# Kernel tuning notes

Hardware: AMD Instinct MI355X
Metric: run time of the kernel (lower is better)

Reference implementation:

```python
import jax, jax.numpy as jnp
import numpy as np

K_HEADS = 8
D_HEAD = 64
D = K_HEADS * D_HEAD  # 512
B, TP, TQ, N = 8, 48, 48, 256


def setup_inputs() -> dict:
    key = jax.random.key(0)
    ks = jax.random.split(key, 13)
    s = 1.0 / np.sqrt(D)
    inp = {
        "X": jax.random.normal(ks[0], (B, TP, N, D), jnp.float32),
        "STE_P": jax.random.normal(ks[1], (B, TP, N, D), jnp.float32),
        "STE_Q": jax.random.normal(ks[2], (B, TQ, N, D), jnp.float32),
        "Wq": jax.random.uniform(ks[3], (D, D), jnp.float32, -s, s),
        "bq": jax.random.uniform(ks[4], (D,), jnp.float32, -s, s),
        "Wk": jax.random.uniform(ks[5], (D, D), jnp.float32, -s, s),
        "bk": jax.random.uniform(ks[6], (D,), jnp.float32, -s, s),
        "Wv": jax.random.uniform(ks[7], (D, D), jnp.float32, -s, s),
        "bv": jax.random.uniform(ks[8], (D,), jnp.float32, -s, s),
        "W1": jax.random.uniform(ks[9], (D, D), jnp.float32, -s, s),
        "b1": jax.random.uniform(ks[10], (D,), jnp.float32, -s, s),
        "W2": jax.random.uniform(ks[11], (D, D), jnp.float32, -s, s),
        "b2": jax.random.uniform(ks[12], (D,), jnp.float32, -s, s),
    }
    return inp


def reference(X, STE_P, STE_Q, Wq, bq, Wk, bk, Wv, bv, W1, b1, W2, b2):
    # ReLU-fused QKV projections
    q = jax.nn.relu(STE_Q @ Wq + bq)  # [B, Tq, N, D]
    k = jax.nn.relu(STE_P @ Wk + bk)  # [B, Tp, N, D]
    v = jax.nn.relu(X @ Wv + bv)      # [B, Tp, N, D]

    # split(last, d) + cat(dim 0) == introduce head axis h of size K
    b, tq, n, _ = q.shape
    tp = k.shape[1]
    q = q.reshape(b, tq, n, K_HEADS, D_HEAD)
    k = k.reshape(b, tp, n, K_HEADS, D_HEAD)
    v = v.reshape(b, tp, n, K_HEADS, D_HEAD)

    # attention over the TIME axis, per node and head: scores [b,h,n,tq,tp]
    scale = 1.0 / jnp.sqrt(jnp.asarray(D_HEAD, q.dtype))
    attn = jnp.einsum('bqnhd,bpnhd->bhnqp', q, k) * scale
    attn = jax.nn.softmax(attn, axis=-1)
    out = jnp.einsum('bhnqp,bpnhd->bqnhd', attn, v).reshape(b, tq, n, D)

    out = jax.nn.relu(out @ W1 + b1) @ W2 + b2
    return out
```

## Files before the change

### kernel.cpp

```cpp
#include <hip/hip_runtime.h>

typedef _Float16 f16;
typedef __fp16 hf2 __attribute__((ext_vector_type(2)));
typedef _Float16 f16x4 __attribute__((ext_vector_type(4)));
typedef _Float16 f16x8 __attribute__((ext_vector_type(8)));
typedef float f32x4 __attribute__((ext_vector_type(4)));

typedef const __attribute__((address_space(1))) unsigned int guint;
typedef __attribute__((address_space(3))) unsigned int luint;
__device__ __forceinline__ void gl_lds16(const void* g, void* l) {
    __builtin_amdgcn_global_load_lds((guint*)g, (luint*)l, 16, 0, 0);
}
template <int N>
__device__ __forceinline__ void vmwait() {
    if constexpr (N == 8)       asm volatile("s_waitcnt vmcnt(8)" ::: "memory");
    else if constexpr (N == 5)  asm volatile("s_waitcnt vmcnt(5)" ::: "memory");
    else if constexpr (N == 4)  asm volatile("s_waitcnt vmcnt(4)" ::: "memory");
    else                        asm volatile("s_waitcnt vmcnt(0)" ::: "memory");
}
__device__ __forceinline__ void barrier_raw() { __builtin_amdgcn_s_barrier(); __builtin_amdgcn_sched_barrier(0); }

__device__ __forceinline__ f16x8 pack8(float4 x0, float4 x1) {
    hf2 p0 = __builtin_amdgcn_cvt_pkrtz(x0.x, x0.y);
    hf2 p1 = __builtin_amdgcn_cvt_pkrtz(x0.z, x0.w);
    hf2 p2 = __builtin_amdgcn_cvt_pkrtz(x1.x, x1.y);
    hf2 p3 = __builtin_amdgcn_cvt_pkrtz(x1.z, x1.w);
    f16x8 h;
    h[0] = (f16)p0[0]; h[1] = (f16)p0[1]; h[2] = (f16)p1[0]; h[3] = (f16)p1[1];
    h[4] = (f16)p2[0]; h[5] = (f16)p2[1]; h[6] = (f16)p3[0]; h[7] = (f16)p3[1];
    return h;
}

__global__ __launch_bounds__(256) void wconv(const float* w0, const float* w1, const float* w2,
                                             const float* w3, const float* w4, f16* dst) {
    const float* src;
    switch (blockIdx.z) { case 0: src = w0; break; case 1: src = w1; break;
                          case 2: src = w2; break; case 3: src = w3; break; default: src = w4; }
    __shared__ float tile[32][33];
    int k0 = blockIdx.x * 32, n0 = blockIdx.y * 32;
    int t = threadIdx.x;
    int r = t >> 3, c4 = (t & 7) * 4;
    float4 v = *(const float4*)(src + (k0 + r) * 512 + n0 + c4);
    tile[r][c4 + 0] = v.x; tile[r][c4 + 1] = v.y; tile[r][c4 + 2] = v.z; tile[r][c4 + 3] = v.w;
    __syncthreads();
    f16x4 o;
    o[0] = (f16)tile[c4 + 0][r]; o[1] = (f16)tile[c4 + 1][r];
    o[2] = (f16)tile[c4 + 2][r]; o[3] = (f16)tile[c4 + 3][r];
    *(f16x4*)(dst + (size_t)blockIdx.z * 262144 + (n0 + r) * 512 + k0 + c4) = o;
}

__global__ __launch_bounds__(256) void conv3(const float* __restrict__ a0, const float* __restrict__ a1,
                                             const float* __restrict__ a2, f16* __restrict__ d0,
                                             f16* __restrict__ d1, f16* __restrict__ d2) {
    const float* s; f16* d;
    if (blockIdx.y == 0)      { s = a0; d = d0; }
    else if (blockIdx.y == 1) { s = a1; d = d1; }
    else                      { s = a2; d = d2; }
    const int n8 = 6291456;
    int i = blockIdx.x * 256 + threadIdx.x;
    const int stride = gridDim.x * 256;
    for (; i < n8; i += stride) {
        const float4* p = (const float4*)(s + (size_t)i * 8);
        float4 x0 = p[0], x1 = p[1];
        *(f16x8*)(d + (size_t)i * 8) = pack8(x0, x1);
    }
}

__global__ __launch_bounds__(512, 1) void gemm_f512(const f16* __restrict__ A,
                                                    const f16* __restrict__ Bt,
                                                    const float* __restrict__ bias,
                                                    f16* __restrict__ Cp) {
    constexpr int ASZ = 8192;
    constexpr int BSZ = 32768;
    constexpr int BUFSZ = ASZ + BSZ;
    __shared__ __align__(16) char smem[3 * BUFSZ];

    const int cpx = gridDim.x >> 3;
    const int orig = blockIdx.x;
    const int bx = (orig & 7) * cpx + (orig >> 3);
    const int r0 = bx * 128;

    const int t = threadIdx.x;
    const int j = t & 63, w = t >> 6;
    const int lr = j & 15, lq = j >> 4;
    const int wr = (w >> 2) * 64, wc = (w & 3) * 128;

    const int sblk = (t & 3) ^ ((t >> 3) & 3);
    const f16* aS = A  + (size_t)(r0 + (t >> 2)) * 512 + sblk * 8;
    const f16* bS = Bt + (size_t)(t >> 2) * 512 + sblk * 8;
    const int dstT = t * 16;

    int aoff[4], boff[8];
#pragma unroll
    for (int m = 0; m < 4; m++) {
        int row = wr + m * 16 + lr;
        aoff[m] = row * 64 + ((lq ^ ((row >> 1) & 3)) << 4);
    }
#pragma unroll
    for (int nb = 0; nb < 8; nb++) {
        int row = wc + nb * 16 + lr;
        boff[nb] = ASZ + row * 64 + ((lq ^ ((row >> 1) & 3)) << 4);
    }

    f32x4 acc[4][8] = {};

    auto stageA = [&](int kt, int buf) {
        gl_lds16(aS + kt * 32, smem + buf * BUFSZ + dstT);
    };
    auto stageB01 = [&](int kt, int buf) {
        char* d = smem + buf * BUFSZ + ASZ + dstT;
        const f16* s = bS + kt * 32;
        gl_lds16(s, d);
        gl_lds16(s + 65536, d + 8192);
    };
    auto stageB23 = [&](int kt, int buf) {
        char* d = smem + buf * BUFSZ + ASZ + dstT;
        const f16* s = bS + kt * 32;
        gl_lds16(s + 131072, d + 16384);
        gl_lds16(s + 196608, d + 24576);
    };

    stageA(0, 0); stageB01(0, 0); stageB23(0, 0);
    stageA(1, 1); stageB01(1, 1); stageB23(1, 1);

    int bufc = 0;
#pragma unroll 1
    for (int kt = 0; kt < 16; ++kt) {
        const char* sb = smem + bufc * BUFSZ;
        const int b1 = (bufc == 2) ? 0 : bufc + 1;
        const int bufs2 = (b1 == 2) ? 0 : b1 + 1;
        if (kt < 15) vmwait<5>(); else vmwait<0>();
        barrier_raw();
        if (kt < 14) { stageA(kt + 2, bufs2); stageB01(kt + 2, bufs2); }
        f16x8 bfr[8], afr[2];
#pragma unroll
        for (int nb = 0; nb < 8; nb++) bfr[nb] = *(const f16x8*)(sb + boff[nb]);
#pragma unroll
        for (int m = 0; m < 2; m++) afr[m] = *(const f16x8*)(sb + aoff[m]);
        __builtin_amdgcn_s_setprio(1);
#pragma unroll
        for (int m = 0; m < 2; m++)
#pragma unroll
            for (int nb = 0; nb < 8; nb++)
                acc[m][nb] = __builtin_amdgcn_mfma_f32_16x16x32_f16(afr[m], bfr[nb], acc[m][nb], 0, 0, 0);
        __builtin_amdgcn_s_setprio(0);
        barrier_raw();
        if (kt < 14) stageB23(kt + 2, bufs2);
        f16x8 afr2[2];
#pragma unroll
        for (int m = 0; m < 2; m++) afr2[m] = *(const f16x8*)(sb + aoff[m + 2]);
        __builtin_amdgcn_s_setprio(1);
#pragma unroll
        for (int m = 0; m < 2; m++)
#pragma unroll
            for (int nb = 0; nb < 8; nb++)
                acc[m + 2][nb] = __builtin_amdgcn_mfma_f32_16x16x32_f16(afr2[m], bfr[nb], acc[m + 2][nb], 0, 0, 0);
        __builtin_amdgcn_s_setprio(0);
        bufc = b1;
    }

#pragma unroll
    for (int nb = 0; nb < 8; nb++) {
        int col = wc + nb * 16 + lr;
        float b = bias[col];
#pragma unroll
        for (int m = 0; m < 4; m++) {
#pragma unroll
            for (int r = 0; r < 4; r++) {
                float v = fmaxf(acc[m][nb][r] + b, 0.0f);
                size_t row = (size_t)(r0 + wr + m * 16 + lq * 4 + r);
                Cp[row * 512 + col] = (f16)v;
            }
        }
    }
}

template <bool RELU, bool O16>
__global__ __launch_bounds__(512, 2) void gemm_8ph(const f16* __restrict__ A,
                                                   const f16* __restrict__ Bt,
                                                   const float* __restrict__ bias,
                                                   void* __restrict__ Cp) {
    constexpr int BUFSZ = 32768;
    __shared__ __align__(16) char smem[4 * BUFSZ];

    const int cpx = gridDim.x >> 3;
    const int orig = blockIdx.x;
    const int wgid = (orig & 7) * cpx + (orig >> 3);
    const int by = wgid & 1;
    const int bx = wgid >> 1;
    const int r0 = bx * 256, c0 = by * 256;

    const int t = threadIdx.x;
    const int j = t & 63, w = t >> 6;
    const int lr = j & 15, lq = j >> 4;
    const int wr = (w >> 2) * 128, wc = (w & 3) * 64;

    const int srow = t >> 2;
    const int sblk = (t & 3) ^ ((t >> 3) & 3);
    const f16* aS = A  + (size_t)(r0 + srow) * 512 + sblk * 8;
    const f16* bS = Bt + (size_t)(c0 + srow) * 512 + sblk * 8;
    const int dstT = t * 16;

    int aoff[8], boff[4];
#pragma unroll
    for (int m = 0; m < 8; m++) {
        int row = wr + m * 16 + lr;
        aoff[m] = row * 64 + ((lq ^ ((row >> 1) & 3)) << 4);
    }
#pragma unroll
    for (int nb = 0; nb < 4; nb++) {
        int row = wc + nb * 16 + lr;
        boff[nb] = 16384 + row * 64 + ((lq ^ ((row >> 1) & 3)) << 4);
    }

    f32x4 acc[8][4] = {};

    auto stageA = [&](int kt) {
        char* d = smem + (kt & 3) * BUFSZ + dstT;
        const f16* s = aS + kt * 32;
        gl_lds16(s, d);
        gl_lds16(s + 65536, d + 8192);
    };
    auto stageB = [&](int kt) {
        char* d = smem + (kt & 3) * BUFSZ + 16384 + dstT;
        const f16* s = bS + kt * 32;
        gl_lds16(s, d);
        gl_lds16(s + 65536, d + 8192);
    };

    stageA(0); stageB(0); stageA(1); stageB(1); stageA(2); stageB(2);

#pragma unroll 1
    for (int kt = 0; kt < 16; ++kt) {
        const char* sb = smem + (kt & 3) * BUFSZ;
        if (kt <= 13)      vmwait<8>();
        else if (kt == 14) vmwait<4>();
        else               vmwait<0>();
        barrier_raw();
        if (kt < 13) stageA(kt + 3);
        f16x8 bfr[4], afr[4];
#pragma unroll
        for (int nb = 0; nb < 4; nb++) bfr[nb] = *(const f16x8*)(sb + boff[nb]);
#pragma unroll
        for (int m = 0; m < 4; m++) afr[m] = *(const f16x8*)(sb + aoff[m]);
        __builtin_amdgcn_s_setprio(1);
#pragma unroll
        for (int m = 0; m < 4; m++)
#pragma unroll
            for (int nb = 0; nb < 4; nb++)
                acc[m][nb] = __builtin_amdgcn_mfma_f32_16x16x32_f16(afr[m], bfr[nb], acc[m][nb], 0, 0, 0);
        __builtin_amdgcn_s_setprio(0);
        barrier_raw();
        if (kt < 13) stageB(kt + 3);
        f16x8 afr2[4];
#pragma unroll
        for (int m = 0; m < 4; m++) afr2[m] = *(const f16x8*)(sb + aoff[m + 4]);
        __builtin_amdgcn_s_setprio(1);
#pragma unroll
        for (int m = 0; m < 4; m++)
#pragma unroll
            for (int nb = 0; nb < 4; nb++)
                acc[m + 4][nb] = __builtin_amdgcn_mfma_f32_16x16x32_f16(afr2[m], bfr[nb], acc[m + 4][nb], 0, 0, 0);
        __builtin_amdgcn_s_setprio(0);
    }

#pragma unroll
    for (int nb = 0; nb < 4; nb++) {
        int col = c0 + wc + nb * 16 + lr;
        float b = bias[col];
#pragma unroll
        for (int m = 0; m < 8; m++) {
#pragma unroll
            for (int r = 0; r < 4; r++) {
                float v = acc[m][nb][r] + b;
                if (RELU) v = fmaxf(v, 0.0f);
                size_t row = (size_t)(r0 + wr + m * 16 + lq * 4 + r);
                if (O16) ((f16*)Cp)[row * 512 + col] = (f16)v;
                else     ((float*)Cp)[row * 512 + col] = v;
            }
        }
    }
}

__global__ __launch_bounds__(64) void attn_kernel(const f16* __restrict__ q,
                                                  const f16* __restrict__ k,
                                                  const f16* __restrict__ v,
                                                  f16* __restrict__ out) {
    const int h = blockIdx.x, n = blockIdx.y, b = blockIdx.z;
    __shared__ f16 sQ[48 * 72];
    __shared__ f16 sK[48 * 72];
    __shared__ f16 sP[48 * 72];
    __shared__ f16 sVt[64 * 72];
    const int l = threadIdx.x, lr = l & 15, lq = l >> 4;
    const size_t rowstride = 256 * 512;
    const size_t base = ((size_t)(b * 48) * 256 + n) * 512 + h * 64;

    const int pr = l >> 3, pc = (l & 7) * 8;
#pragma unroll
    for (int pass = 0; pass < 6; pass++) {
        int row = pass * 8 + pr;
        size_t g = base + (size_t)row * rowstride + pc;
        f16x8 qv = *(const f16x8*)(q + g);
        f16x8 kv = *(const f16x8*)(k + g);
        f16x8 vv = *(const f16x8*)(v + g);
        *(f16x8*)&sQ[row * 72 + pc] = qv;
        *(f16x8*)&sK[row * 72 + pc] = kv;
#pragma unroll
        for (int jj = 0; jj < 8; jj++) sVt[(pc + jj) * 72 + row] = vv[jj];
    }
    {
        f16x8 z = {};
        *(f16x8*)&sVt[l * 72 + 48] = z;
        *(f16x8*)&sVt[l * 72 + 56] = z;
        if (l < 48) { *(f16x8*)&sP[l * 72 + 48] = z; *(f16x8*)&sP[l * 72 + 56] = z; }
    }
    __syncthreads();

    f32x4 s[3][3] = {};
#pragma unroll
    for (int ks = 0; ks < 2; ks++) {
        f16x8 aq[3], bk[3];
#pragma unroll
        for (int m = 0; m < 3; m++)  aq[m] = *(const f16x8*)&sQ[(m * 16 + lr) * 72 + ks * 32 + lq * 8];
#pragma unroll
        for (int nb = 0; nb < 3; nb++) bk[nb] = *(const f16x8*)&sK[(nb * 16 + lr) * 72 + ks * 32 + lq * 8];
#pragma unroll
        for (int m = 0; m < 3; m++)
#pragma unroll
            for (int nb = 0; nb < 3; nb++)
                s[m][nb] = __builtin_amdgcn_mfma_f32_16x16x32_f16(aq[m], bk[nb], s[m][nb], 0, 0, 0);
    }

#pragma unroll
    for (int m = 0; m < 3; m++) {
#pragma unroll
        for (int r = 0; r < 4; r++) {
            float a0 = s[m][0][r] * 0.125f, a1 = s[m][1][r] * 0.125f, a2 = s[m][2][r] * 0.125f;
            float mx = fmaxf(a0, fmaxf(a1, a2));
#pragma unroll
            for (int d = 1; d < 16; d <<= 1) mx = fmaxf(mx, __shfl_xor(mx, d));
            float e0 = __expf(a0 - mx), e1 = __expf(a1 - mx), e2 = __expf(a2 - mx);
            float sm = e0 + e1 + e2;
#pragma unroll
            for (int d = 1; d < 16; d <<= 1) sm += __shfl_xor(sm, d);
            float inv = 1.0f / sm;
            int row = m * 16 + lq * 4 + r;
            sP[row * 72 + 0  + lr] = (f16)(e0 * inv);
            sP[row * 72 + 16 + lr] = (f16)(e1 * inv);
            sP[row * 72 + 32 + lr] = (f16)(e2 * inv);
        }
    }
    __syncthreads();

    f32x4 o[3][4] = {};
#pragma unroll
    for (int ks = 0; ks < 2; ks++) {
        f16x8 ap[3], bvv[4];
#pragma unroll
        for (int m = 0; m < 3; m++)  ap[m] = *(const f16x8*)&sP[(m * 16 + lr) * 72 + ks * 32 + lq * 8];
#pragma unroll
        for (int nb = 0; nb < 4; nb++) bvv[nb] = *(const f16x8*)&sVt[(nb * 16 + lr) * 72 + ks * 32 + lq * 8];
#pragma unroll
        for (int m = 0; m < 3; m++)
#pragma unroll
            for (int nb = 0; nb < 4; nb++)
                o[m][nb] = __builtin_amdgcn_mfma_f32_16x16x32_f16(ap[m], bvv[nb], o[m][nb], 0, 0, 0);
    }

#pragma unroll
    for (int m = 0; m < 3; m++)
#pragma unroll
        for (int nb = 0; nb < 4; nb++)
#pragma unroll
            for (int r = 0; r < 4; r++) {
                int row = m * 16 + lq * 4 + r;
                out[base + (size_t)row * rowstride + nb * 16 + lr] = (f16)o[m][nb][r];
            }
}

extern "C" void kernel_launch(void* const* d_in, const int* in_sizes, int n_in,
                              void* d_out, int out_size, void* d_ws, size_t ws_size,
                              hipStream_t stream) {
    const float* X    = (const float*)d_in[0];
    const float* STEP = (const float*)d_in[1];
    const float* STEQ = (const float*)d_in[2];
    const float* Wq   = (const float*)d_in[3];
    const float* bq   = (const float*)d_in[4];
    const float* Wk   = (const float*)d_in[5];
    const float* bk   = (const float*)d_in[6];
    const float* Wv   = (const float*)d_in[7];
    const float* bv   = (const float*)d_in[8];
    const float* W1   = (const float*)d_in[9];
    const float* b1   = (const float*)d_in[10];
    const float* W2   = (const float*)d_in[11];
    const float* b2   = (const float*)d_in[12];
    float* out = (float*)d_out;

    const size_t MROWS = 98304;
    f16* ws  = (f16*)d_ws;
    f16* Wqt = ws;
    f16* Wkt = ws + 262144;
    f16* Wvt = ws + 524288;
    f16* W1t = ws + 786432;
    f16* W2t = ws + 1048576;
    f16* qb  = ws + 1310720;
    f16* kb  = qb + MROWS * 512;
    f16* vb  = kb + MROWS * 512;
    f16* hb  = kb;

    wconv<<<dim3(16, 16, 5), 256, 0, stream>>>(Wq, Wk, Wv, W1, W2, ws);

    conv3<<<dim3(2048, 3), 256, 0, stream>>>(STEQ, STEP, X, qb, kb, vb);

    gemm_f512<<<768, 512, 0, stream>>>(qb, Wqt, bq, qb);
    gemm_f512<<<768, 512, 0, stream>>>(kb, Wkt, bk, kb);
    gemm_f512<<<768, 512, 0, stream>>>(vb, Wvt, bv, vb);

    attn_kernel<<<dim3(8, 256, 8), 64, 0, stream>>>(qb, kb, vb, qb);

    gemm_8ph<true,  true ><<<768, 512, 0, stream>>>(qb, W1t, b1, hb);
    gemm_8ph<false, false><<<768, 512, 0, stream>>>(hb, W2t, b2, out);
}
```

Before: 696.6 us.

## Replace in-place QKV GEMMs with 256x256-tile 8-phase GEMM using output buffer as staging

Removes the in-place 128-row gemm_f512 projection kernel and runs the Q/K/V projections with the 256x256-tile gemm_8ph body. Q and K are batched into one two-slice launch, and V gets its own launch. Because the 8-phase GEMM cannot write in place, the fp16-converted inputs are staged in the output buffer, and the conversion kernel is unrolled 4x across a grid stride. The aim is better operand reuse and occupancy than the single-wave-per-CU 128-row kernel. It adds an extra conversion launch and relies on the output buffer being large enough to hold two fp16 staging copies.

```diff
diff --git a/kernel.cpp b/kernel.cpp
--- a/kernel.cpp
+++ b/kernel.cpp
@@ -14,7 +14,6 @@
 template <int N>
 __device__ __forceinline__ void vmwait() {
     if constexpr (N == 8)       asm volatile("s_waitcnt vmcnt(8)" ::: "memory");
-    else if constexpr (N == 5)  asm volatile("s_waitcnt vmcnt(5)" ::: "memory");
     else if constexpr (N == 4)  asm volatile("s_waitcnt vmcnt(4)" ::: "memory");
     else                        asm volatile("s_waitcnt vmcnt(0)" ::: "memory");
 }
@@ -49,142 +48,37 @@
     *(f16x4*)(dst + (size_t)blockIdx.z * 262144 + (n0 + r) * 512 + k0 + c4) = o;
 }
 
-__global__ __launch_bounds__(256) void conv3(const float* __restrict__ a0, const float* __restrict__ a1,
-                                             const float* __restrict__ a2, f16* __restrict__ d0,
-                                             f16* __restrict__ d1, f16* __restrict__ d2) {
-    const float* s; f16* d;
-    if (blockIdx.y == 0)      { s = a0; d = d0; }
-    else if (blockIdx.y == 1) { s = a1; d = d1; }
-    else                      { s = a2; d = d2; }
+__global__ __launch_bounds__(256) void convert2(const float* __restrict__ a0, const float* __restrict__ a1,
+                                                f16* __restrict__ d0, f16* __restrict__ d1) {
+    const float* __restrict__ s = (blockIdx.y == 0) ? a0 : a1;
+    f16* __restrict__ d        = (blockIdx.y == 0) ? d0 : d1;
     const int n8 = 6291456;
+    const int span = gridDim.x * 256;
     int i = blockIdx.x * 256 + threadIdx.x;
-    const int stride = gridDim.x * 256;
-    for (; i < n8; i += stride) {
-        const float4* p = (const float4*)(s + (size_t)i * 8);
-        float4 x0 = p[0], x1 = p[1];
-        *(f16x8*)(d + (size_t)i * 8) = pack8(x0, x1);
-    }
-}
-
-__global__ __launch_bounds__(512, 1) void gemm_f512(const f16* __restrict__ A,
-                                                    const f16* __restrict__ Bt,
-                                                    const float* __restrict__ bias,
-                                                    f16* __restrict__ Cp) {
-    constexpr int ASZ = 8192;
-    constexpr int BSZ = 32768;
-    constexpr int BUFSZ = ASZ + BSZ;
-    __shared__ __align__(16) char smem[3 * BUFSZ];
-
-    const int cpx = gridDim.x >> 3;
-    const int orig = blockIdx.x;
-    const int bx = (orig & 7) * cpx + (orig >> 3);
-    const int r0 = bx * 128;
-
-    const int t = threadIdx.x;
-    const int j = t & 63, w = t >> 6;
-    const int lr = j & 15, lq = j >> 4;
-    const int wr = (w >> 2) * 64, wc = (w & 3) * 128;
-
-    const int sblk = (t & 3) ^ ((t >> 3) & 3);
-    const f16* aS = A  + (size_t)(r0 + (t >> 2)) * 512 + sblk * 8;
-    const f16* bS = Bt + (size_t)(t >> 2) * 512 + sblk * 8;
-    const int dstT = t * 16;
-
-    int aoff[4], boff[8];
-#pragma unroll
-    for (int m = 0; m < 4; m++) {
-        int row = wr + m * 16 + lr;
-        aoff[m] = row * 64 + ((lq ^ ((row >> 1) & 3)) << 4);
-    }
-#pragma unroll
-    for (int nb = 0; nb < 8; nb++) {
-        int row = wc + nb * 16 + lr;
-        boff[nb] = ASZ + row * 64 + ((lq ^ ((row >> 1) & 3)) << 4);
-    }
-
-    f32x4 acc[4][8] = {};
-
-    auto stageA = [&](int kt, int buf) {
-        gl_lds16(aS + kt * 32, smem + buf * BUFSZ + dstT);
-    };
-    auto stageB01 = [&](int kt, int buf) {
-        char* d = smem + buf * BUFSZ + ASZ + dstT;
-        const f16* s = bS + kt * 32;
-        gl_lds16(s, d);
-        gl_lds16(s + 65536, d + 8192);
-    };
-    auto stageB23 = [&](int kt, int buf) {
-        char* d = smem + buf * BUFSZ + ASZ + dstT;
-        const f16* s = bS + kt * 32;
-        gl_lds16(s + 131072, d + 16384);
-        gl_lds16(s + 196608, d + 24576);
-    };
-
-    stageA(0, 0); stageB01(0, 0); stageB23(0, 0);
-    stageA(1, 1); stageB01(1, 1); stageB23(1, 1);
-
-    int bufc = 0;
 #pragma unroll 1
-    for (int kt = 0; kt < 16; ++kt) {
-        const char* sb = smem + bufc * BUFSZ;
-        const int b1 = (bufc == 2) ? 0 : bufc + 1;
-        const int bufs2 = (b1 == 2) ? 0 : b1 + 1;
-        if (kt < 15) vmwait<5>(); else vmwait<0>();
-        barrier_raw();
-        if (kt < 14) { stageA(kt + 2, bufs2); stageB01(kt + 2, bufs2); }
-        f16x8 bfr[8], afr[2];
-#pragma unroll
-        for (int nb = 0; nb < 8; nb++) bfr[nb] = *(const f16x8*)(sb + boff[nb]);
-#pragma unroll
-        for (int m = 0; m < 2; m++) afr[m] = *(const f16x8*)(sb + aoff[m]);
-        __builtin_amdgcn_s_setprio(1);
-#pragma unroll
-        for (int m = 0; m < 2; m++)
-#pragma unroll
-            for (int nb = 0; nb < 8; nb++)
-                acc[m][nb] = __builtin_amdgcn_mfma_f32_16x16x32_f16(afr[m], bfr[nb], acc[m][nb], 0, 0, 0);
-        __builtin_amdgcn_s_setprio(0);
-        barrier_raw();
-        if (kt < 14) stageB23(kt + 2, bufs2);
-        f16x8 afr2[2];
-#pragma unroll
-        for (int m = 0; m < 2; m++) afr2[m] = *(const f16x8*)(sb + aoff[m + 2]);
-        __builtin_amdgcn_s_setprio(1);
-#pragma unroll
-        for (int m = 0; m < 2; m++)
-#pragma unroll
-            for (int nb = 0; nb < 8; nb++)
-                acc[m + 2][nb] = __builtin_amdgcn_mfma_f32_16x16x32_f16(afr2[m], bfr[nb], acc[m + 2][nb], 0, 0, 0);
-        __builtin_amdgcn_s_setprio(0);
-        bufc = b1;
-    }
-
-#pragma unroll
-    for (int nb = 0; nb < 8; nb++) {
-        int col = wc + nb * 16 + lr;
-        float b = bias[col];
-#pragma unroll
-        for (int m = 0; m < 4; m++) {
-#pragma unroll
-            for (int r = 0; r < 4; r++) {
-                float v = fmaxf(acc[m][nb][r] + b, 0.0f);
-                size_t row = (size_t)(r0 + wr + m * 16 + lq * 4 + r);
-                Cp[row * 512 + col] = (f16)v;
-            }
-        }
+    for (; i < n8; i += 4 * span) {
+        const float4* p0 = (const float4*)(s + (size_t)i * 8);
+        const float4* p1 = (const float4*)(s + (size_t)(i + span) * 8);
+        const float4* p2 = (const float4*)(s + (size_t)(i + 2 * span) * 8);
+        const float4* p3 = (const float4*)(s + (size_t)(i + 3 * span) * 8);
+        float4 a0_ = p0[0], b0_ = p0[1];
+        float4 a1_ = p1[0], b1_ = p1[1];
+        float4 a2_ = p2[0], b2_ = p2[1];
+        float4 a3_ = p3[0], b3_ = p3[1];
+        *(f16x8*)(d + (size_t)i * 8)              = pack8(a0_, b0_);
+        *(f16x8*)(d + (size_t)(i + span) * 8)     = pack8(a1_, b1_);
+        *(f16x8*)(d + (size_t)(i + 2 * span) * 8) = pack8(a2_, b2_);
+        *(f16x8*)(d + (size_t)(i + 3 * span) * 8) = pack8(a3_, b3_);
     }
 }
 
 template <bool RELU, bool O16>
-__global__ __launch_bounds__(512, 2) void gemm_8ph(const f16* __restrict__ A,
-                                                   const f16* __restrict__ Bt,
-                                                   const float* __restrict__ bias,
-                                                   void* __restrict__ Cp) {
+__device__ __forceinline__ void g8_body(char* smem, const f16* __restrict__ A, const f16* __restrict__ Bt,
+                                        const float* __restrict__ bias, void* __restrict__ Cp,
+                                        int nwgx, int orig) {
     constexpr int BUFSZ = 32768;
-    __shared__ __align__(16) char smem[4 * BUFSZ];
-
-    const int cpx = gridDim.x >> 3;
-    const int orig = blockIdx.x;
+
+    const int cpx = nwgx >> 3;
     const int wgid = (orig & 7) * cpx + (orig >> 3);
     const int by = wgid & 1;
     const int bx = wgid >> 1;
@@ -280,6 +174,20 @@
             }
         }
     }
+}
+
+template <bool RELU, bool O16>
+__global__ __launch_bounds__(512, 2) void gemm_8ph(const f16* __restrict__ A, const f16* __restrict__ Bt,
+                                                   const float* __restrict__ bias, void* __restrict__ Cp) {
+    __shared__ __align__(16) char smem[131072];
+    g8_body<RELU, O16>(smem, A, Bt, bias, Cp, gridDim.x, blockIdx.x);
+}
+
+__global__ __launch_bounds__(512, 2) void g8_pair(const f16* A0, const f16* B0, const float* b0, f16* C0,
+                                                  const f16* A1, const f16* B1, const float* b1, f16* C1) {
+    __shared__ __align__(16) char smem[131072];
+    if (blockIdx.z == 0) g8_body<true, true>(smem, A0, B0, b0, C0, gridDim.x, blockIdx.x);
+    else                 g8_body<true, true>(smem, A1, B1, b1, C1, gridDim.x, blockIdx.x);
 }
 
 __global__ __launch_bounds__(64) void attn_kernel(const f16* __restrict__ q,
@@ -397,6 +305,7 @@
     float* out = (float*)d_out;
 
     const size_t MROWS = 98304;
+    const size_t MBUF  = MROWS * 512;
     f16* ws  = (f16*)d_ws;
     f16* Wqt = ws;
     f16* Wkt = ws + 262144;
@@ -404,17 +313,21 @@
     f16* W1t = ws + 786432;
     f16* W2t = ws + 1048576;
     f16* qb  = ws + 1310720;
-    f16* kb  = qb + MROWS * 512;
-    f16* vb  = kb + MROWS * 512;
+    f16* kb  = qb + MBUF;
+    f16* vb  = kb + MBUF;
     f16* hb  = kb;
 
+    f16* s0 = (f16*)d_out;
+    f16* s1 = s0 + MBUF;
+
     wconv<<<dim3(16, 16, 5), 256, 0, stream>>>(Wq, Wk, Wv, W1, W2, ws);
 
-    conv3<<<dim3(2048, 3), 256, 0, stream>>>(STEQ, STEP, X, qb, kb, vb);
-
-    gemm_f512<<<768, 512, 0, stream>>>(qb, Wqt, bq, qb);
-    gemm_f512<<<768, 512, 0, stream>>>(kb, Wkt, bk, kb);
-    gemm_f512<<<768, 512, 0, stream>>>(vb, Wvt, bv, vb);
+    convert2<<<dim3(1024, 2), 256, 0, stream>>>(STEQ, STEP, s0, s1);
+
+    g8_pair<<<dim3(768, 1, 2), 512, 0, stream>>>(s0, Wqt, bq, qb, s1, Wkt, bk, kb);
+
+    convert2<<<dim3(1024, 1), 256, 0, stream>>>(X, X, s0, s0);
+    gemm_8ph<true, true><<<768, 512, 0, stream>>>(s0, Wvt, bv, vb);
 
     attn_kernel<<<dim3(8, 256, 8), 64, 0, stream>>>(qb, kb, vb, qb);
 
```

Result: slower. 757.4 us (+8.7%).
